# Optimization experiments

Measured on AMD Instinct MI355X. Metric: run time of the kernel, lower is better.

Reference implementation:

```python
import jax, jax.numpy as jnp
import numpy as np

B, N_INST, H, W = 8, 64, 480, 480
EPS = 1e-12  # torch F.normalize eps


def setup_inputs() -> dict:
    key = jax.random.key(0)
    k1, k2, k3, k4, k5, k6 = jax.random.split(key, 6)
    # binary instance masks (output of connected-component labeling in the original)
    instance_masks = (jax.random.uniform(k1, (N_INST, H, W)) < 0.3).astype(jnp.float32)
    sample_ids = jax.random.randint(k2, (N_INST,), 0, B, dtype=jnp.int64)
    quaternion = jax.random.normal(k3, (B, 4, H, W), dtype=jnp.float32)
    scales = jax.random.normal(k4, (B, 3, H, W), dtype=jnp.float32)
    xy = jax.random.normal(k5, (B, 2, H, W), dtype=jnp.float32)
    z = jax.random.normal(k6, (B, H, W), dtype=jnp.float32)
    return {"instance_masks": instance_masks, "sample_ids": sample_ids,
            "quaternion": quaternion, "scales": scales, "xy": xy, "z": z}


def reference(instance_masks, sample_ids, quaternion, scales, xy, z):
    # instance_masks: [N,H,W] binary float; sample_ids: [N] in [0,B)
    mask_size = jnp.sum(instance_masks, axis=(-2, -1))  # [N]

    def masked_mean(d):  # d: [N,C,H,W] -> [N,C]
        return jnp.einsum('nhw,nchw->nc', instance_masks, d) / mask_size[:, None]

    # quaternion: masked mean then L2-normalize along channel dim
    q_agg = masked_mean(quaternion[sample_ids])                       # [N,4]
    q_agg = q_agg / jnp.maximum(jnp.linalg.norm(q_agg, axis=1, keepdims=True), EPS)
    # scales: masked mean
    s_agg = masked_mean(scales[sample_ids])                           # [N,3]
    # z: masked mean of [N,1,H,W] then exp
    z_agg = jnp.exp(masked_mean(z[sample_ids][:, None]))              # [N,1]
    # xy: masked dense map (passed on to hough voting downstream)
    xy_masked = instance_masks[:, None] * xy[sample_ids]              # [N,2,H,W]
    return q_agg, s_agg, z_agg, xy_masked
```

## Files before the change

### kernel.cpp

```cpp
#include <hip/hip_runtime.h>
#include <math.h>

#define HW      (480 * 480)
#define HW4     (HW / 4)
#define NINST   64
#define NB      8
#define NV      9
#define GI      8
#define NBLK    225
#define THREADS 256

__device__ __forceinline__ float dot4(const float4 a, const float4 b) {
    return (a.x * b.x + a.y * b.y) + (a.z * b.z + a.w * b.w);
}

template <int CTRL>
__device__ __forceinline__ float dpp_add(float x) {
    int s = __builtin_amdgcn_update_dpp(0, __float_as_int(x), CTRL, 0xf, 0xf, false);
    return x + __int_as_float(s);
}
__device__ __forceinline__ float wave_sum(float x) {
    x = dpp_add<0x111>(x);
    x = dpp_add<0x112>(x);
    x = dpp_add<0x114>(x);
    x = dpp_add<0x118>(x);
    x = dpp_add<0x142>(x);
    x = dpp_add<0x143>(x);
    return x;
}

__global__ __launch_bounds__(THREADS) void agg_main(
    const float* __restrict__ masks,
    const int*   __restrict__ sids,
    const float* __restrict__ quat,
    const float* __restrict__ scales,
    const float* __restrict__ xy,
    const float* __restrict__ z,
    float*       __restrict__ out,
    float*       __restrict__ part)
{
    const int tid = threadIdx.x;
    const int bx  = blockIdx.x;
    const int b   = blockIdx.y;
    const int i   = bx * THREADS + tid;

    __shared__ int   ilist[NINST];
    __shared__ int   scnt;
    __shared__ float swred[4][GI * NV];

    if (tid == 0) {
        int c = 0;
        for (int n = 0; n < NINST; ++n)
            if (sids[n] == b) ilist[c++] = n;
        scnt = c;
    }
    __syncthreads();
    const int cnt = scnt;

    const float4* M  = (const float4*)masks;
    const float4* Q  = (const float4*)quat   + (size_t)b * 4 * HW4;
    const float4* S  = (const float4*)scales + (size_t)b * 3 * HW4;
    const float4* X  = (const float4*)xy     + (size_t)b * 2 * HW4;
    const float4* Zp = (const float4*)z      + (size_t)b * HW4;
    float4*       O  = (float4*)(out + 512);

    const float4 vq0 = Q[0 * HW4 + i];
    const float4 vq1 = Q[1 * HW4 + i];
    const float4 vq2 = Q[2 * HW4 + i];
    const float4 vq3 = Q[3 * HW4 + i];
    const float4 vs0 = S[0 * HW4 + i];
    const float4 vs1 = S[1 * HW4 + i];
    const float4 vs2 = S[2 * HW4 + i];
    const float4 vx0 = X[0 * HW4 + i];
    const float4 vx1 = X[1 * HW4 + i];
    const float4 vz  = Zp[i];

    const int lane = tid & 63;
    const int wid  = tid >> 6;

    for (int g0 = 0; g0 < cnt; g0 += GI) {
        int  nidx[GI];
        bool valid[GI];
#pragma unroll
        for (int j = 0; j < GI; ++j) {
            valid[j] = (g0 + j < cnt);
            nidx[j]  = ilist[valid[j] ? (g0 + j) : (cnt - 1)];
        }

        float4 m[GI];
#pragma unroll
        for (int j = 0; j < GI; ++j)
            m[j] = M[(size_t)nidx[j] * HW4 + i];

#pragma unroll
        for (int j = 0; j < GI; ++j) {
            if (valid[j]) {
                O[((size_t)nidx[j] * 2 + 0) * HW4 + i] = make_float4(
                    m[j].x * vx0.x, m[j].y * vx0.y, m[j].z * vx0.z, m[j].w * vx0.w);
                O[((size_t)nidx[j] * 2 + 1) * HW4 + i] = make_float4(
                    m[j].x * vx1.x, m[j].y * vx1.y, m[j].z * vx1.z, m[j].w * vx1.w);
            }
        }

        float acc[GI][NV];
#pragma unroll
        for (int j = 0; j < GI; ++j) {
            acc[j][0] = (m[j].x + m[j].y) + (m[j].z + m[j].w);
            acc[j][1] = dot4(m[j], vq0);
            acc[j][2] = dot4(m[j], vq1);
            acc[j][3] = dot4(m[j], vq2);
            acc[j][4] = dot4(m[j], vq3);
            acc[j][5] = dot4(m[j], vs0);
            acc[j][6] = dot4(m[j], vs1);
            acc[j][7] = dot4(m[j], vs2);
            acc[j][8] = dot4(m[j], vz);
        }

#pragma unroll
        for (int j = 0; j < GI; ++j)
#pragma unroll
            for (int v = 0; v < NV; ++v) {
                const float t = wave_sum(acc[j][v]);
                if (lane == 63) swred[wid][j * NV + v] = t;
            }
        __syncthreads();
        if (tid < GI * NV) {
            const int j = tid / NV;
            const int v = tid - j * NV;
            if (g0 + j < cnt) {
                const int n = ilist[g0 + j];
                part[((size_t)n * NBLK + bx) * NV + v] =
                    (swred[0][tid] + swred[1][tid]) + (swred[2][tid] + swred[3][tid]);
            }
        }
        __syncthreads();
    }
}

__global__ __launch_bounds__(THREADS) void agg_final(
    const float* __restrict__ part,
    float*       __restrict__ out)
{
    const int n   = blockIdx.x;
    const int tid = threadIdx.x;

    float vals[NV];
#pragma unroll
    for (int v = 0; v < NV; ++v) vals[v] = 0.0f;
    for (int c = tid; c < NBLK; c += THREADS) {
        const float* p = part + ((size_t)n * NBLK + c) * NV;
#pragma unroll
        for (int v = 0; v < NV; ++v) vals[v] += p[v];
    }

    __shared__ float sred[4][NV];
    const int lane = tid & 63;
    const int wid  = tid >> 6;
#pragma unroll
    for (int v = 0; v < NV; ++v) {
        float x = vals[v];
#pragma unroll
        for (int off = 32; off > 0; off >>= 1)
            x += __shfl_down(x, off, 64);
        if (lane == 0) sred[wid][v] = x;
    }
    __syncthreads();

    if (tid == 0) {
        float s[NV];
#pragma unroll
        for (int v = 0; v < NV; ++v)
            s[v] = (sred[0][v] + sred[1][v]) + (sred[2][v] + sred[3][v]);

        const float inv = 1.0f / s[0];
        const float q0 = s[1] * inv, q1 = s[2] * inv, q2 = s[3] * inv, q3 = s[4] * inv;
        const float norm = sqrtf(q0 * q0 + q1 * q1 + q2 * q2 + q3 * q3);
        const float d = fmaxf(norm, 1e-12f);
        out[n * 4 + 0] = q0 / d;
        out[n * 4 + 1] = q1 / d;
        out[n * 4 + 2] = q2 / d;
        out[n * 4 + 3] = q3 / d;

        out[256 + n * 3 + 0] = s[5] * inv;
        out[256 + n * 3 + 1] = s[6] * inv;
        out[256 + n * 3 + 2] = s[7] * inv;

        out[448 + n] = expf(s[8] * inv);
    }
}

extern "C" void kernel_launch(void* const* d_in, const int* in_sizes, int n_in,
                              void* d_out, int out_size, void* d_ws, size_t ws_size,
                              hipStream_t stream) {
    const float* masks  = (const float*)d_in[0];
    const int*   sids   = (const int*)d_in[1];
    const float* quat   = (const float*)d_in[2];
    const float* scales = (const float*)d_in[3];
    const float* xy     = (const float*)d_in[4];
    const float* z      = (const float*)d_in[5];
    float* out  = (float*)d_out;
    float* part = (float*)d_ws;

    dim3 grid(NBLK, NB);
    agg_main<<<grid, THREADS, 0, stream>>>(masks, sids, quat, scales, xy, z, out, part);
    agg_final<<<NINST, THREADS, 0, stream>>>(part, out);
}
```

Before: 245.7 us.

## Process three pixel tiles per block to amortize reductions, with nontemporal output stores

Each block now covers three 256-pixel float4 tiles per instance group, accumulating per-thread partials across the tiles before the wave/block reduction. This cuts the block count and the reduction and sync work per pixel by a factor of three, and shrinks the partials array read by the final kernel. Per-batch data is reloaded inside the tile loop instead of being held for the whole kernel, so it is re-read once per instance group. The xy_masked output uses nontemporal stores to avoid cache pollution, the instance list is built with a wave ballot, and launch bounds ask for two blocks per SIMD, which may raise register pressure or cause spills.

Result: slower. 253.1 us (+3.0%).

```diff
diff --git a/kernel.cpp b/kernel.cpp
--- a/kernel.cpp
+++ b/kernel.cpp
@@ -7,8 +7,11 @@
 #define NB      8
 #define NV      9
 #define GI      8
-#define NBLK    225
+#define ITER    3
+#define NBLK    75
 #define THREADS 256
+
+typedef float f4 __attribute__((ext_vector_type(4)));
 
 __device__ __forceinline__ float dot4(const float4 a, const float4 b) {
     return (a.x * b.x + a.y * b.y) + (a.z * b.z + a.w * b.w);
@@ -29,7 +32,7 @@
     return x;
 }
 
-__global__ __launch_bounds__(THREADS) void agg_main(
+__global__ __launch_bounds__(THREADS, 2) void agg_main(
     const float* __restrict__ masks,
     const int*   __restrict__ sids,
     const float* __restrict__ quat,
@@ -42,17 +45,19 @@
     const int tid = threadIdx.x;
     const int bx  = blockIdx.x;
     const int b   = blockIdx.y;
-    const int i   = bx * THREADS + tid;
 
     __shared__ int   ilist[NINST];
     __shared__ int   scnt;
     __shared__ float swred[4][GI * NV];
 
-    if (tid == 0) {
-        int c = 0;
-        for (int n = 0; n < NINST; ++n)
-            if (sids[n] == b) ilist[c++] = n;
-        scnt = c;
+    if (tid < 64) {
+        const bool mine = (sids[tid] == b);
+        const unsigned long long mk = __ballot(mine);
+        if (mine) {
+            const int rank = __popcll(mk & ((1ull << tid) - 1ull));
+            ilist[rank] = tid;
+        }
+        if (tid == 0) scnt = __popcll(mk);
     }
     __syncthreads();
     const int cnt = scnt;
@@ -62,18 +67,7 @@
     const float4* S  = (const float4*)scales + (size_t)b * 3 * HW4;
     const float4* X  = (const float4*)xy     + (size_t)b * 2 * HW4;
     const float4* Zp = (const float4*)z      + (size_t)b * HW4;
-    float4*       O  = (float4*)(out + 512);
-
-    const float4 vq0 = Q[0 * HW4 + i];
-    const float4 vq1 = Q[1 * HW4 + i];
-    const float4 vq2 = Q[2 * HW4 + i];
-    const float4 vq3 = Q[3 * HW4 + i];
-    const float4 vs0 = S[0 * HW4 + i];
-    const float4 vs1 = S[1 * HW4 + i];
-    const float4 vs2 = S[2 * HW4 + i];
-    const float4 vx0 = X[0 * HW4 + i];
-    const float4 vx1 = X[1 * HW4 + i];
-    const float4 vz  = Zp[i];
+    f4*           O  = (f4*)(out + 512);
 
     const int lane = tid & 63;
     const int wid  = tid >> 6;
@@ -87,33 +81,55 @@
             nidx[j]  = ilist[valid[j] ? (g0 + j) : (cnt - 1)];
         }
 
-        float4 m[GI];
+        float acc[GI][NV];
 #pragma unroll
         for (int j = 0; j < GI; ++j)
-            m[j] = M[(size_t)nidx[j] * HW4 + i];
-
-#pragma unroll
-        for (int j = 0; j < GI; ++j) {
-            if (valid[j]) {
-                O[((size_t)nidx[j] * 2 + 0) * HW4 + i] = make_float4(
-                    m[j].x * vx0.x, m[j].y * vx0.y, m[j].z * vx0.z, m[j].w * vx0.w);
-                O[((size_t)nidx[j] * 2 + 1) * HW4 + i] = make_float4(
-                    m[j].x * vx1.x, m[j].y * vx1.y, m[j].z * vx1.z, m[j].w * vx1.w);
-            }
-        }
-
-        float acc[GI][NV];
-#pragma unroll
-        for (int j = 0; j < GI; ++j) {
-            acc[j][0] = (m[j].x + m[j].y) + (m[j].z + m[j].w);
-            acc[j][1] = dot4(m[j], vq0);
-            acc[j][2] = dot4(m[j], vq1);
-            acc[j][3] = dot4(m[j], vq2);
-            acc[j][4] = dot4(m[j], vq3);
-            acc[j][5] = dot4(m[j], vs0);
-            acc[j][6] = dot4(m[j], vs1);
-            acc[j][7] = dot4(m[j], vs2);
-            acc[j][8] = dot4(m[j], vz);
+#pragma unroll
+            for (int v = 0; v < NV; ++v) acc[j][v] = 0.0f;
+
+#pragma unroll
+        for (int it = 0; it < ITER; ++it) {
+            const int i = (bx * ITER + it) * THREADS + tid;
+
+            float4 m[GI];
+#pragma unroll
+            for (int j = 0; j < GI; ++j)
+                m[j] = M[(size_t)nidx[j] * HW4 + i];
+            const float4 vq0 = Q[0 * HW4 + i];
+            const float4 vq1 = Q[1 * HW4 + i];
+            const float4 vq2 = Q[2 * HW4 + i];
+            const float4 vq3 = Q[3 * HW4 + i];
+            const float4 vs0 = S[0 * HW4 + i];
+            const float4 vs1 = S[1 * HW4 + i];
+            const float4 vs2 = S[2 * HW4 + i];
+            const float4 vx0 = X[0 * HW4 + i];
+            const float4 vx1 = X[1 * HW4 + i];
+            const float4 vz  = Zp[i];
+
+#pragma unroll
+            for (int j = 0; j < GI; ++j) {
+                if (valid[j]) {
+                    f4 o0 = { m[j].x * vx0.x, m[j].y * vx0.y,
+                              m[j].z * vx0.z, m[j].w * vx0.w };
+                    f4 o1 = { m[j].x * vx1.x, m[j].y * vx1.y,
+                              m[j].z * vx1.z, m[j].w * vx1.w };
+                    __builtin_nontemporal_store(o0, &O[((size_t)nidx[j] * 2 + 0) * HW4 + i]);
+                    __builtin_nontemporal_store(o1, &O[((size_t)nidx[j] * 2 + 1) * HW4 + i]);
+                }
+            }
+
+#pragma unroll
+            for (int j = 0; j < GI; ++j) {
+                acc[j][0] += (m[j].x + m[j].y) + (m[j].z + m[j].w);
+                acc[j][1] += dot4(m[j], vq0);
+                acc[j][2] += dot4(m[j], vq1);
+                acc[j][3] += dot4(m[j], vq2);
+                acc[j][4] += dot4(m[j], vq3);
+                acc[j][5] += dot4(m[j], vs0);
+                acc[j][6] += dot4(m[j], vs1);
+                acc[j][7] += dot4(m[j], vs2);
+                acc[j][8] += dot4(m[j], vz);
+            }
         }
 
 #pragma unroll
```
